# Kernel optimization log

Hardware: AMD Instinct MI355X
Metric: run time of the kernel (lower is better)

## Reference

```python
import jax, jax.numpy as jnp
import numpy as np

N, D, H, L = 50000, 128, 4, 3
E = 800000
C = D // H            # head dim = 32
NEG_SLOPE = 0.2       # PyG GATv2Conv default negative_slope
LN_EPS = 1e-5         # nn.LayerNorm default eps


def setup_inputs() -> dict:
    key = jax.random.key(0)
    ks = jax.random.split(key, 8)
    s = 1.0 / np.sqrt(D).astype(np.float32)
    return {
        "fine_poi_x": jax.random.normal(ks[0], (N, D), jnp.float32),
        "edge_index": jax.random.randint(ks[1], (2, E), 0, N, dtype=jnp.int32),
        "Wl": jax.random.normal(ks[2], (L, D, D), jnp.float32) * s,
        "bl": jnp.zeros((L, D), jnp.float32),
        "Wr": jax.random.normal(ks[3], (L, D, D), jnp.float32) * s,
        "br": jnp.zeros((L, D), jnp.float32),
        "att": jax.random.normal(ks[4], (L, H, C), jnp.float32) * s,
        "bias": jnp.zeros((L, D), jnp.float32),
        "gamma": jnp.ones((L, D), jnp.float32),
        "beta": jnp.zeros((L, D), jnp.float32),
    }


def _gatv2_conv(x, src, dst, Wl, bl, Wr, br, att, bias):
    # x: [N, D]; src/dst: [E'] (self-loops already appended)
    xl = (x @ Wl + bl).reshape(N, H, C)   # source-side transform (lin_l)
    xr = (x @ Wr + br).reshape(N, H, C)   # target-side transform (lin_r)
    m = xl[src] + xr[dst]                 # [E', H, C] per-edge pre-activation
    m = jax.nn.leaky_relu(m, NEG_SLOPE)
    e = jnp.einsum("ehc,hc->eh", m, att)  # [E', H] attention logits
    # segment softmax over edges grouped by destination node
    emax = jax.ops.segment_max(e, dst, num_segments=N)      # [N, H]
    ee = jnp.exp(e - emax[dst])
    denom = jax.ops.segment_sum(ee, dst, num_segments=N)    # [N, H]
    alpha = ee / denom[dst]               # self-loops guarantee denom >= 1 term
    out = jax.ops.segment_sum(xl[src] * alpha[:, :, None], dst, num_segments=N)
    return out.reshape(N, D) + bias


def _layernorm(x, g, b):
    mu = jnp.mean(x, axis=-1, keepdims=True)
    var = jnp.var(x, axis=-1, keepdims=True)
    return (x - mu) * jax.lax.rsqrt(var + LN_EPS) * g + b


def reference(fine_poi_x, edge_index, Wl, bl, Wr, br, att, bias, gamma, beta):
    # PyG GATv2Conv add_self_loops=True: append i->i edges
    loops = jnp.arange(N, dtype=edge_index.dtype)
    src = jnp.concatenate([edge_index[0], loops])
    dst = jnp.concatenate([edge_index[1], loops])
    x = fine_poi_x
    for i in range(L):
        h = _gatv2_conv(x, src, dst, Wl[i], bl[i], Wr[i], br[i], att[i], bias[i])
        x = _layernorm(x + h, gamma[i], beta[i])
        if i != L - 1:
            x = jax.nn.relu(x)
    return x
```

## Files before the change

kernel.cpp:

```cpp
#include <hip/hip_runtime.h>

#define N_NODES 50000
#define N_EDGES 800000
#define DIM 128
#define TOT_EDGES (N_EDGES + N_NODES)
#define LOG2E 1.44269504088896f

#define BSHIFT 9
#define BNODES 512
#define NB ((N_NODES + BNODES - 1) / BNODES)
#define BCAP 16384
#define EPB 4096
#define EPT 16
#define NBLK_A ((TOT_EDGES + EPB - 1) / EPB)

typedef __attribute__((ext_vector_type(8))) _Float16 f16x8;
typedef __attribute__((ext_vector_type(2))) _Float16 h2;
typedef __attribute__((ext_vector_type(4))) float f32x4;
typedef decltype(__builtin_amdgcn_cvt_pkrtz(0.f, 0.f)) fp16v2;

__device__ inline uint h2u(h2 v) { return __builtin_bit_cast(uint, v); }
__device__ inline h2 u2h(uint v) { return __builtin_bit_cast(h2, v); }
__device__ inline uint pk2u(fp16v2 v) { return __builtin_bit_cast(uint, v); }

__device__ inline float rowsum16(float v) {
  int x;
  x = __builtin_amdgcn_update_dpp(0, __float_as_int(v), 0x128, 0xF, 0xF, true);
  v += __int_as_float(x);
  x = __builtin_amdgcn_update_dpp(0, __float_as_int(v), 0x124, 0xF, 0xF, true);
  v += __int_as_float(x);
  x = __builtin_amdgcn_update_dpp(0, __float_as_int(v), 0x122, 0xF, 0xF, true);
  v += __int_as_float(x);
  x = __builtin_amdgcn_update_dpp(0, __float_as_int(v), 0x121, 0xF, 0xF, true);
  v += __int_as_float(x);
  return v;
}

__device__ inline float quadsum4(float v) {
  int x;
  x = __builtin_amdgcn_update_dpp(0, __float_as_int(v), 0xB1, 0xF, 0xF, true);
  v += __int_as_float(x);
  x = __builtin_amdgcn_update_dpp(0, __float_as_int(v), 0x4E, 0xF, 0xF, true);
  v += __int_as_float(x);
  return v;
}


__global__ __launch_bounds__(256) void convx_kernel(const float* __restrict__ x,
                                                    uint* __restrict__ xb,
                                                    int* __restrict__ bcnt) {
  if (blockIdx.x == 0 && threadIdx.x < NB) bcnt[threadIdx.x] = 0;
  int t = blockIdx.x * 256 + threadIdx.x;
  if (t < N_NODES * (DIM / 2)) {
    float2 v = ((const float2*)x)[t];
    xb[t] = pk2u(__builtin_amdgcn_cvt_pkrtz(v.x, v.y));
  }
}

__global__ __launch_bounds__(256) void convwa_kernel(const float* __restrict__ Wl,
                                                     const float* __restrict__ Wr,
                                                     ushort* __restrict__ Wt,
                                                     const float* __restrict__ att,
                                                     uint* __restrict__ attc,
                                                     uint* __restrict__ col) {
  int t = blockIdx.x * 256 + threadIdx.x;
  if (blockIdx.x == 0) {
    int u = threadIdx.x;
    if (u < 192) {
      float a0 = att[2 * u] * LOG2E, a1 = att[2 * u + 1] * LOG2E;
      attc[u] = pk2u(__builtin_amdgcn_cvt_pkrtz(a0, a1));
    }
    if (u < 64) col[TOT_EDGES + u] = 0u;
  }
  if (t >= 3 * 2 * DIM * DIM) return;
  int k = t & 127;
  int n = (t >> 7) & 127;
  int w = (t >> 14) & 1;
  int l = t >> 15;
  const float* W = w ? Wr : Wl;
  _Float16 h = (_Float16)W[l * DIM * DIM + k * DIM + n];
  Wt[t] = __builtin_bit_cast(ushort, h);
}


__global__ __launch_bounds__(256) void partA_kernel(const int* __restrict__ srcArr,
                                                    const int* __restrict__ dstArr,
                                                    int* __restrict__ bcnt,
                                                    uint2* __restrict__ bbuf) {
  int tid = threadIdx.x;
  int e0 = blockIdx.x * EPB;
  __shared__ int hist[NB], base[NB], loff[NB];
  if (tid < NB) { hist[tid] = 0; loff[tid] = 0; }
  __syncthreads();

  int sv[EPT], dv[EPT];
#pragma unroll
  for (int i = 0; i < EPT; ++i) {
    int e = e0 + i * 256 + tid;
    int s = 0, d = -1;
    if (e < TOT_EDGES) {
      if (e < N_EDGES) { s = srcArr[e]; d = dstArr[e]; }
      else { s = e - N_EDGES; d = s; }
    }
    sv[i] = s; dv[i] = d;
    if (d >= 0) atomicAdd(&hist[d >> BSHIFT], 1);
  }
  __syncthreads();
  if (tid < NB) {
    int h = hist[tid];
    if (h > 0) base[tid] = atomicAdd(&bcnt[tid], h);
  }
  __syncthreads();
#pragma unroll
  for (int i = 0; i < EPT; ++i) {
    int d = dv[i];
    if (d >= 0) {
      int b = d >> BSHIFT;
      int p = atomicAdd(&loff[b], 1);
      bbuf[(size_t)b * BCAP + base[b] + p] = make_uint2((uint)sv[i], (uint)d);
    }
  }
}


__global__ __launch_bounds__(512) void partB_kernel(const uint2* __restrict__ bbuf,
                                                    const int* __restrict__ bcnt,
                                                    int* __restrict__ rowptr,
                                                    uint* __restrict__ col) {
  int b = blockIdx.x, tid = threadIdx.x;

  __shared__ int s[128];
  if (tid < 128) s[tid] = (tid < NB) ? bcnt[tid] : 0;
  __syncthreads();
  for (int off = 1; off < 128; off <<= 1) {
    int t = 0;
    if (tid < 128 && tid >= off) t = s[tid - off];
    __syncthreads();
    if (tid < 128) s[tid] += t;
    __syncthreads();
  }
  int cb = (b > 0) ? s[b - 1] : 0;
  int m = bcnt[b];
  if (b == 0 && tid == 0) rowptr[N_NODES] = TOT_EDGES;
  const uint2* buf = bbuf + (size_t)b * BCAP;

  __shared__ int cnt[BNODES], scn[BNODES], cur[BNODES];
  cnt[tid] = 0;
  __syncthreads();
  for (int e = tid; e < m; e += 512) {
    int d = (int)buf[e].y;
    atomicAdd(&cnt[d & (BNODES - 1)], 1);
  }
  __syncthreads();
  int c = cnt[tid];
  scn[tid] = c;
  __syncthreads();
  for (int off = 1; off < BNODES; off <<= 1) {
    int t = (tid >= off) ? scn[tid - off] : 0;
    __syncthreads();
    scn[tid] += t;
    __syncthreads();
  }
  int excl = scn[tid] - c;
  int node = b * BNODES + tid;
  if (node < N_NODES) rowptr[node] = cb + excl;
  cur[tid] = excl;
  __syncthreads();
  for (int e = tid; e < m; e += 512) {
    uint2 sd = buf[e];
    int p = atomicAdd(&cur[(int)sd.y & (BNODES - 1)], 1);
    col[cb + p] = sd.x * 16u;
  }
}


__global__ __launch_bounds__(256) void gemm_mfma_kernel(
    const uint* __restrict__ xb,
    const ushort* __restrict__ Wt,
    const float* __restrict__ bl, const float* __restrict__ br,
    uint* __restrict__ xl, uint* __restrict__ xr) {
  int wave = threadIdx.x >> 6, lane = threadIdx.x & 63;
  int lr = lane & 15, kq = lane >> 4;
  int m0 = blockIdx.x * 64;

  const ushort* W = Wt + (wave >> 1) * (DIM * DIM);
  const float* bias = (wave >> 1) ? br : bl;
  uint* outp = (wave >> 1) ? xr : xl;
  int n0 = (wave & 1) * 64;
  const ushort* xbp = (const ushort*)xb;

  f16x8 bfrag[4][4];
#pragma unroll
  for (int nt = 0; nt < 4; ++nt)
#pragma unroll
    for (int kt = 0; kt < 4; ++kt)
      bfrag[nt][kt] = *(const f16x8*)(W + (n0 + nt * 16 + lr) * DIM + kt * 32 + kq * 8);

  f32x4 acc[4][4];
#pragma unroll
  for (int mt = 0; mt < 4; ++mt)
#pragma unroll
    for (int nt = 0; nt < 4; ++nt)
      acc[mt][nt] = (f32x4){0.f, 0.f, 0.f, 0.f};

  f16x8 af[4];
  {
    int m = m0 + lr;
    int mc = m < N_NODES ? m : N_NODES - 1;
#pragma unroll
    for (int kt = 0; kt < 4; ++kt)
      af[kt] = *(const f16x8*)(xbp + (size_t)mc * DIM + kt * 32 + kq * 8);
  }
#pragma unroll
  for (int mt = 0; mt < 4; ++mt) {
    f16x8 afn[4];
    if (mt < 3) {
      int m2 = m0 + (mt + 1) * 16 + lr;
      int mc2 = m2 < N_NODES ? m2 : N_NODES - 1;
#pragma unroll
      for (int kt = 0; kt < 4; ++kt)
        afn[kt] = *(const f16x8*)(xbp + (size_t)mc2 * DIM + kt * 32 + kq * 8);
    }
#pragma unroll
    for (int nt = 0; nt < 4; ++nt)
#pragma unroll
      for (int kt = 0; kt < 4; ++kt)
        acc[mt][nt] = __builtin_amdgcn_mfma_f32_16x16x32_f16(bfrag[nt][kt], af[kt],
                                                             acc[mt][nt], 0, 0, 0);
    if (mt < 3) {
      af[0] = afn[0]; af[1] = afn[1]; af[2] = afn[2]; af[3] = afn[3];
    }
  }

#pragma unroll
  for (int mt = 0; mt < 4; ++mt) {
    int m = m0 + mt * 16 + lr;
    if (m < N_NODES) {
#pragma unroll
      for (int nt = 0; nt < 4; ++nt) {
        int n = n0 + nt * 16 + kq * 4;
        float4 bb = *(const float4*)(bias + n);
        uint2 o;
        o.x = pk2u(__builtin_amdgcn_cvt_pkrtz(acc[mt][nt][0] + bb.x, acc[mt][nt][1] + bb.y));
        o.y = pk2u(__builtin_amdgcn_cvt_pkrtz(acc[mt][nt][2] + bb.z, acc[mt][nt][3] + bb.w));
        *(uint2*)(outp + (size_t)m * (DIM / 2) + (n >> 1)) = o;
      }
    }
  }
}


__global__ __launch_bounds__(64) void att_kernel(
    const uint4* __restrict__ xinb, const uint4* __restrict__ xlb,
    const uint4* __restrict__ xrb, const int* __restrict__ rowptr,
    const uint* __restrict__ col, const uint4* __restrict__ attc,
    const float4* __restrict__ bias, const float4* __restrict__ gamma,
    const float4* __restrict__ beta, uint4* __restrict__ xoutb,
    float4* __restrict__ xoutf, int do_relu) {
  int lane = threadIdx.x;
  uint j = (uint)(lane & 15);
  int e4 = lane >> 4;
  int n = blockIdx.x;

  uint4 rq = xrb[(uint)(n * 16) + j];
  uint4 aq = attc[j];
  h2 r2[4] = {u2h(rq.x), u2h(rq.y), u2h(rq.z), u2h(rq.w)};
  h2 at2[4] = {u2h(aq.x), u2h(aq.y), u2h(aq.z), u2h(aq.w)};
  const h2 c02 = {(_Float16)0.2f, (_Float16)0.2f};

  h2 accp[4] = {};
  float den = 0.f;

  int js = rowptr[n], je = rowptr[n + 1];

  uint cA = col[(uint)(js + e4)];
  uint cB = col[(uint)(js + 4 + e4)];
  uint cC = col[(uint)(js + 8 + e4)];
  uint4 gA = xlb[cA + j];
  uint4 gB = xlb[cB + j];

  for (int cbase = js; cbase < je; cbase += 4) {
    uint cD = col[(uint)(cbase + 12 + e4)];
    uint4 gC = xlb[cC + j];

    h2 a0 = u2h(gA.x), a1 = u2h(gA.y), a2 = u2h(gA.z), a3 = u2h(gA.w);
    float p = 0.f;
    {
      h2 s0 = a0 + r2[0], s1 = a1 + r2[1], s2 = a2 + r2[2], s3 = a3 + r2[3];
      h2 m0 = __builtin_elementwise_max(s0, s0 * c02);
      h2 m1 = __builtin_elementwise_max(s1, s1 * c02);
      h2 m2 = __builtin_elementwise_max(s2, s2 * c02);
      h2 m3 = __builtin_elementwise_max(s3, s3 * c02);
      p = __builtin_amdgcn_fdot2(__builtin_bit_cast(fp16v2, m0),
                                 __builtin_bit_cast(fp16v2, at2[0]), p, false);
      p = __builtin_amdgcn_fdot2(__builtin_bit_cast(fp16v2, m1),
                                 __builtin_bit_cast(fp16v2, at2[1]), p, false);
      p = __builtin_amdgcn_fdot2(__builtin_bit_cast(fp16v2, m2),
                                 __builtin_bit_cast(fp16v2, at2[2]), p, false);
      p = __builtin_amdgcn_fdot2(__builtin_bit_cast(fp16v2, m3),
                                 __builtin_bit_cast(fp16v2, at2[3]), p, false);
    }
    p = quadsum4(p);
    float w = (cbase + e4 < je) ? __builtin_amdgcn_exp2f(p) : 0.f;
    den += w;
    _Float16 wh = (_Float16)w;
    h2 w2 = {wh, wh};
    accp[0] = w2 * a0 + accp[0];
    accp[1] = w2 * a1 + accp[1];
    accp[2] = w2 * a2 + accp[2];
    accp[3] = w2 * a3 + accp[3];

    gA = gB; gB = gC; cC = cD;
  }

#pragma unroll
  for (int t = 0; t < 4; ++t) {
    accp[t] += u2h((uint)__shfl_xor((int)h2u(accp[t]), 16, 64));
    accp[t] += u2h((uint)__shfl_xor((int)h2u(accp[t]), 32, 64));
  }
  den += __shfl_xor(den, 16, 64);
  den += __shfl_xor(den, 32, 64);

  float inv = 1.0f / den;
  float acc[8];
#pragma unroll
  for (int t = 0; t < 4; ++t) {
    acc[2 * t] = (float)accp[t].x;
    acc[2 * t + 1] = (float)accp[t].y;
  }

  uint4 xi4 = xinb[(uint)(n * 16) + j];
  h2 xi[4] = {u2h(xi4.x), u2h(xi4.y), u2h(xi4.z), u2h(xi4.w)};
  float4 b0 = bias[2 * j], b1 = bias[2 * j + 1];

  float o[8];
  o[0] = fmaf(acc[0], inv, b0.x + (float)xi[0].x);
  o[1] = fmaf(acc[1], inv, b0.y + (float)xi[0].y);
  o[2] = fmaf(acc[2], inv, b0.z + (float)xi[1].x);
  o[3] = fmaf(acc[3], inv, b0.w + (float)xi[1].y);
  o[4] = fmaf(acc[4], inv, b1.x + (float)xi[2].x);
  o[5] = fmaf(acc[5], inv, b1.y + (float)xi[2].y);
  o[6] = fmaf(acc[6], inv, b1.z + (float)xi[3].x);
  o[7] = fmaf(acc[7], inv, b1.w + (float)xi[3].y);

  float s1 = 0.f, s2 = 0.f;
#pragma unroll
  for (int t = 0; t < 8; ++t) { s1 += o[t]; s2 = fmaf(o[t], o[t], s2); }
  s1 = rowsum16(s1);
  s2 = rowsum16(s2);
  float mean = s1 * (1.0f / DIM);
  float var = s2 * (1.0f / DIM) - mean * mean;
  float rstd = rsqrtf(var + 1e-5f);

  float4 g0 = gamma[2 * j], g1 = gamma[2 * j + 1];
  float4 t0 = beta[2 * j], t1 = beta[2 * j + 1];
  float y[8];
  y[0] = (o[0] - mean) * rstd * g0.x + t0.x;
  y[1] = (o[1] - mean) * rstd * g0.y + t0.y;
  y[2] = (o[2] - mean) * rstd * g0.z + t0.z;
  y[3] = (o[3] - mean) * rstd * g0.w + t0.w;
  y[4] = (o[4] - mean) * rstd * g1.x + t1.x;
  y[5] = (o[5] - mean) * rstd * g1.y + t1.y;
  y[6] = (o[6] - mean) * rstd * g1.z + t1.z;
  y[7] = (o[7] - mean) * rstd * g1.w + t1.w;
  if (do_relu) {
#pragma unroll
    for (int t = 0; t < 8; ++t) y[t] = fmaxf(y[t], 0.f);
  }

  if (e4 == 0) {
    if (xoutb) {
      uint4 ov;
      ov.x = pk2u(__builtin_amdgcn_cvt_pkrtz(y[0], y[1]));
      ov.y = pk2u(__builtin_amdgcn_cvt_pkrtz(y[2], y[3]));
      ov.z = pk2u(__builtin_amdgcn_cvt_pkrtz(y[4], y[5]));
      ov.w = pk2u(__builtin_amdgcn_cvt_pkrtz(y[6], y[7]));
      xoutb[(uint)(n * 16) + j] = ov;
    }
    if (xoutf) {
      xoutf[(uint)(n * 32) + 2 * j] = make_float4(y[0], y[1], y[2], y[3]);
      xoutf[(uint)(n * 32) + 2 * j + 1] = make_float4(y[4], y[5], y[6], y[7]);
    }
  }
}


extern "C" void kernel_launch(void* const* d_in, const int* in_sizes, int n_in,
                              void* d_out, int out_size, void* d_ws, size_t ws_size,
                              hipStream_t stream) {
  const float* x_in  = (const float*)d_in[0];
  const int*   eidx  = (const int*)d_in[1];
  const float* Wl    = (const float*)d_in[2];
  const float* bl    = (const float*)d_in[3];
  const float* Wr    = (const float*)d_in[4];
  const float* br    = (const float*)d_in[5];
  const float* att   = (const float*)d_in[6];
  const float* bias  = (const float*)d_in[7];
  const float* gamma = (const float*)d_in[8];
  const float* beta  = (const float*)d_in[9];
  float* out = (float*)d_out;

  char* p = (char*)d_ws;
  auto alloc = [&](size_t bytes) {
    char* q = p;
    p += (bytes + 255) & ~(size_t)255;
    return q;
  };
  uint*  xb       = (uint*)alloc((size_t)N_NODES * (DIM / 2) * 4);
  uint*  xlb      = (uint*)alloc((size_t)N_NODES * (DIM / 2) * 4);
  uint*  xrb      = (uint*)alloc((size_t)N_NODES * (DIM / 2) * 4);
  ushort* Wt      = (ushort*)alloc((size_t)3 * 2 * DIM * DIM * 2);
  uint*  attc     = (uint*)alloc((size_t)3 * 64 * 4);
  int*   rowptr   = (int*)alloc((size_t)(N_NODES + 1) * 4);
  uint*  col      = (uint*)alloc((size_t)(TOT_EDGES + 64) * 4);
  uint2* bbuf     = (uint2*)alloc((size_t)NB * BCAP * 8);
  int*   bcnt     = (int*)alloc((size_t)NB * 4);

  convx_kernel<<<(N_NODES * (DIM / 2) + 255) / 256, 256, 0, stream>>>(x_in, xb, bcnt);
  convwa_kernel<<<(3 * 2 * DIM * DIM + 255) / 256, 256, 0, stream>>>(Wl, Wr, Wt, att, attc, col);
  partA_kernel<<<NBLK_A, 256, 0, stream>>>(eidx, eidx + N_EDGES, bcnt, bbuf);
  partB_kernel<<<NB, 512, 0, stream>>>(bbuf, bcnt, rowptr, col);

  for (int l = 0; l < 3; ++l) {
    gemm_mfma_kernel<<<(N_NODES + 63) / 64, 256, 0, stream>>>(
        xb, Wt + (size_t)l * 2 * DIM * DIM, bl + l * DIM, br + l * DIM, xlb, xrb);
    att_kernel<<<N_NODES, 64, 0, stream>>>(
        (const uint4*)xb, (const uint4*)xlb, (const uint4*)xrb, rowptr, col,
        (const uint4*)(attc + l * 64), (const float4*)(bias + l * DIM),
        (const float4*)(gamma + l * DIM), (const float4*)(beta + l * DIM),
        (l == 2) ? nullptr : (uint4*)xb, (l == 2) ? (float4*)out : nullptr,
        (l != 2) ? 1 : 0);
  }
}
```

Baseline: 240.0 us.

## Merge conversion kernels, pack bucket entries into 32 bits, deepen gather prefetch

Merges the x and weight conversion kernels into a single launch by splitting the grid between the two jobs. Bucket-partition entries are packed into one 32-bit word (source index shifted left by 9, local destination in the low bits), which halves the bbuf write and read traffic. The attention kernel's gather pipeline is deepened from two to five rows of xl in flight, with col indices fetched further ahead, to hide gather latency. The deeper prefetch costs more registers and reads further past each node's edge range. Those extra reads now extend up to 28 entries past the edge array, while only 64 padding entries are zeroed.

```diff
diff --git a/kernel.cpp b/kernel.cpp
--- a/kernel.cpp
+++ b/kernel.cpp
@@ -13,6 +13,8 @@
 #define EPB 4096
 #define EPT 16
 #define NBLK_A ((TOT_EDGES + EPB - 1) / EPB)
+#define CONVX_BLOCKS ((N_NODES * (DIM / 2) + 255) / 256)
+#define CONVW_BLOCKS ((3 * 2 * DIM * DIM + 255) / 256)
 
 typedef __attribute__((ext_vector_type(8))) _Float16 f16x8;
 typedef __attribute__((ext_vector_type(2))) _Float16 h2;
@@ -46,47 +48,51 @@
 }
 
 
-__global__ __launch_bounds__(256) void convx_kernel(const float* __restrict__ x,
-                                                    uint* __restrict__ xb,
-                                                    int* __restrict__ bcnt) {
-  if (blockIdx.x == 0 && threadIdx.x < NB) bcnt[threadIdx.x] = 0;
-  int t = blockIdx.x * 256 + threadIdx.x;
-  if (t < N_NODES * (DIM / 2)) {
-    float2 v = ((const float2*)x)[t];
-    xb[t] = pk2u(__builtin_amdgcn_cvt_pkrtz(v.x, v.y));
-  }
-}
-
-__global__ __launch_bounds__(256) void convwa_kernel(const float* __restrict__ Wl,
-                                                     const float* __restrict__ Wr,
-                                                     ushort* __restrict__ Wt,
-                                                     const float* __restrict__ att,
-                                                     uint* __restrict__ attc,
-                                                     uint* __restrict__ col) {
-  int t = blockIdx.x * 256 + threadIdx.x;
-  if (blockIdx.x == 0) {
-    int u = threadIdx.x;
-    if (u < 192) {
-      float a0 = att[2 * u] * LOG2E, a1 = att[2 * u + 1] * LOG2E;
-      attc[u] = pk2u(__builtin_amdgcn_cvt_pkrtz(a0, a1));
-    }
-    if (u < 64) col[TOT_EDGES + u] = 0u;
-  }
-  if (t >= 3 * 2 * DIM * DIM) return;
-  int k = t & 127;
-  int n = (t >> 7) & 127;
-  int w = (t >> 14) & 1;
-  int l = t >> 15;
-  const float* W = w ? Wr : Wl;
-  _Float16 h = (_Float16)W[l * DIM * DIM + k * DIM + n];
-  Wt[t] = __builtin_bit_cast(ushort, h);
+__global__ __launch_bounds__(256) void conv_kernel(const float* __restrict__ x,
+                                                   uint* __restrict__ xb,
+                                                   int* __restrict__ bcnt,
+                                                   const float* __restrict__ Wl,
+                                                   const float* __restrict__ Wr,
+                                                   ushort* __restrict__ Wt,
+                                                   const float* __restrict__ att,
+                                                   uint* __restrict__ attc,
+                                                   uint* __restrict__ col) {
+  int b = blockIdx.x;
+  if (b < CONVX_BLOCKS) {
+    if (b == 0 && threadIdx.x < NB) bcnt[threadIdx.x] = 0;
+    int t = b * 256 + threadIdx.x;
+    if (t < N_NODES * (DIM / 2)) {
+      float2 v = ((const float2*)x)[t];
+      xb[t] = pk2u(__builtin_amdgcn_cvt_pkrtz(v.x, v.y));
+    }
+  } else {
+    int bb = b - CONVX_BLOCKS;
+    if (bb == 0) {
+      int u = threadIdx.x;
+      if (u < 192) {
+        float a0 = att[2 * u] * LOG2E, a1 = att[2 * u + 1] * LOG2E;
+        attc[u] = pk2u(__builtin_amdgcn_cvt_pkrtz(a0, a1));
+      }
+      if (u < 64) col[TOT_EDGES + u] = 0u;
+    }
+    int t = bb * 256 + threadIdx.x;
+    if (t < 3 * 2 * DIM * DIM) {
+      int k = t & 127;
+      int n = (t >> 7) & 127;
+      int w = (t >> 14) & 1;
+      int l = t >> 15;
+      const float* W = w ? Wr : Wl;
+      _Float16 h = (_Float16)W[l * DIM * DIM + k * DIM + n];
+      Wt[t] = __builtin_bit_cast(ushort, h);
+    }
+  }
 }
 
 
 __global__ __launch_bounds__(256) void partA_kernel(const int* __restrict__ srcArr,
                                                     const int* __restrict__ dstArr,
                                                     int* __restrict__ bcnt,
-                                                    uint2* __restrict__ bbuf) {
+                                                    uint* __restrict__ bbuf) {
   int tid = threadIdx.x;
   int e0 = blockIdx.x * EPB;
   __shared__ int hist[NB], base[NB], loff[NB];
@@ -117,13 +123,13 @@
     if (d >= 0) {
       int b = d >> BSHIFT;
       int p = atomicAdd(&loff[b], 1);
-      bbuf[(size_t)b * BCAP + base[b] + p] = make_uint2((uint)sv[i], (uint)d);
-    }
-  }
-}
-
-
-__global__ __launch_bounds__(512) void partB_kernel(const uint2* __restrict__ bbuf,
+      bbuf[(size_t)b * BCAP + base[b] + p] = ((uint)sv[i] << 9) | (uint)(d & (BNODES - 1));
+    }
+  }
+}
+
+
+__global__ __launch_bounds__(512) void partB_kernel(const uint* __restrict__ bbuf,
                                                     const int* __restrict__ bcnt,
                                                     int* __restrict__ rowptr,
                                                     uint* __restrict__ col) {
@@ -142,14 +148,13 @@
   int cb = (b > 0) ? s[b - 1] : 0;
   int m = bcnt[b];
   if (b == 0 && tid == 0) rowptr[N_NODES] = TOT_EDGES;
-  const uint2* buf = bbuf + (size_t)b * BCAP;
+  const uint* buf = bbuf + (size_t)b * BCAP;
 
   __shared__ int cnt[BNODES], scn[BNODES], cur[BNODES];
   cnt[tid] = 0;
   __syncthreads();
   for (int e = tid; e < m; e += 512) {
-    int d = (int)buf[e].y;
-    atomicAdd(&cnt[d & (BNODES - 1)], 1);
+    atomicAdd(&cnt[buf[e] & (BNODES - 1)], 1);
   }
   __syncthreads();
   int c = cnt[tid];
@@ -167,9 +172,9 @@
   cur[tid] = excl;
   __syncthreads();
   for (int e = tid; e < m; e += 512) {
-    uint2 sd = buf[e];
-    int p = atomicAdd(&cur[(int)sd.y & (BNODES - 1)], 1);
-    col[cb + p] = sd.x * 16u;
+    uint sd = buf[e];
+    int p = atomicAdd(&cur[sd & (BNODES - 1)], 1);
+    col[cb + p] = (sd >> 9) << 4;
   }
 }
 
@@ -273,17 +278,24 @@
 
   int js = rowptr[n], je = rowptr[n + 1];
 
-  uint cA = col[(uint)(js + e4)];
-  uint cB = col[(uint)(js + 4 + e4)];
-  uint cC = col[(uint)(js + 8 + e4)];
-  uint4 gA = xlb[cA + j];
-  uint4 gB = xlb[cB + j];
+  uint c0 = col[(uint)(js + e4)];
+  uint c1 = col[(uint)(js + 4 + e4)];
+  uint c2 = col[(uint)(js + 8 + e4)];
+  uint c3 = col[(uint)(js + 12 + e4)];
+  uint c4 = col[(uint)(js + 16 + e4)];
+  uint c5 = col[(uint)(js + 20 + e4)];
+  uint c6 = col[(uint)(js + 24 + e4)];
+  uint4 g0 = xlb[c0 + j];
+  uint4 g1 = xlb[c1 + j];
+  uint4 g2 = xlb[c2 + j];
+  uint4 g3 = xlb[c3 + j];
+  uint4 g4 = xlb[c4 + j];
 
   for (int cbase = js; cbase < je; cbase += 4) {
-    uint cD = col[(uint)(cbase + 12 + e4)];
-    uint4 gC = xlb[cC + j];
-
-    h2 a0 = u2h(gA.x), a1 = u2h(gA.y), a2 = u2h(gA.z), a3 = u2h(gA.w);
+    uint cn = col[(uint)(cbase + 28 + e4)];
+    uint4 gn = xlb[c5 + j];
+
+    h2 a0 = u2h(g0.x), a1 = u2h(g0.y), a2 = u2h(g0.z), a3 = u2h(g0.w);
     float p = 0.f;
     {
       h2 s0 = a0 + r2[0], s1 = a1 + r2[1], s2 = a2 + r2[2], s3 = a3 + r2[3];
@@ -310,7 +322,8 @@
     accp[2] = w2 * a2 + accp[2];
     accp[3] = w2 * a3 + accp[3];
 
-    gA = gB; gB = gC; cC = cD;
+    g0 = g1; g1 = g2; g2 = g3; g3 = g4; g4 = gn;
+    c5 = c6; c6 = cn;
   }
 
 #pragma unroll
@@ -352,17 +365,17 @@
   float var = s2 * (1.0f / DIM) - mean * mean;
   float rstd = rsqrtf(var + 1e-5f);
 
-  float4 g0 = gamma[2 * j], g1 = gamma[2 * j + 1];
+  float4 g0_ = gamma[2 * j], g1_ = gamma[2 * j + 1];
   float4 t0 = beta[2 * j], t1 = beta[2 * j + 1];
   float y[8];
-  y[0] = (o[0] - mean) * rstd * g0.x + t0.x;
-  y[1] = (o[1] - mean) * rstd * g0.y + t0.y;
-  y[2] = (o[2] - mean) * rstd * g0.z + t0.z;
-  y[3] = (o[3] - mean) * rstd * g0.w + t0.w;
-  y[4] = (o[4] - mean) * rstd * g1.x + t1.x;
-  y[5] = (o[5] - mean) * rstd * g1.y + t1.y;
-  y[6] = (o[6] - mean) * rstd * g1.z + t1.z;
-  y[7] = (o[7] - mean) * rstd * g1.w + t1.w;
+  y[0] = (o[0] - mean) * rstd * g0_.x + t0.x;
+  y[1] = (o[1] - mean) * rstd * g0_.y + t0.y;
+  y[2] = (o[2] - mean) * rstd * g0_.z + t0.z;
+  y[3] = (o[3] - mean) * rstd * g0_.w + t0.w;
+  y[4] = (o[4] - mean) * rstd * g1_.x + t1.x;
+  y[5] = (o[5] - mean) * rstd * g1_.y + t1.y;
+  y[6] = (o[6] - mean) * rstd * g1_.z + t1.z;
+  y[7] = (o[7] - mean) * rstd * g1_.w + t1.w;
   if (do_relu) {
 #pragma unroll
     for (int t = 0; t < 8; ++t) y[t] = fmaxf(y[t], 0.f);
@@ -413,11 +426,11 @@
   uint*  attc     = (uint*)alloc((size_t)3 * 64 * 4);
   int*   rowptr   = (int*)alloc((size_t)(N_NODES + 1) * 4);
   uint*  col      = (uint*)alloc((size_t)(TOT_EDGES + 64) * 4);
-  uint2* bbuf     = (uint2*)alloc((size_t)NB * BCAP * 8);
+  uint*  bbuf     = (uint*)alloc((size_t)NB * BCAP * 4);
   int*   bcnt     = (int*)alloc((size_t)NB * 4);
 
-  convx_kernel<<<(N_NODES * (DIM / 2) + 255) / 256, 256, 0, stream>>>(x_in, xb, bcnt);
-  convwa_kernel<<<(3 * 2 * DIM * DIM + 255) / 256, 256, 0, stream>>>(Wl, Wr, Wt, att, attc, col);
+  conv_kernel<<<CONVX_BLOCKS + CONVW_BLOCKS, 256, 0, stream>>>(
+      x_in, xb, bcnt, Wl, Wr, Wt, att, attc, col);
   partA_kernel<<<NBLK_A, 256, 0, stream>>>(eidx, eidx + N_EDGES, bcnt, bbuf);
   partB_kernel<<<NB, 512, 0, stream>>>(bbuf, bcnt, rowptr, col);
 
```

Measured after the change: 238.9 us (median of 2 runs). Within noise of the previous version (-0.4%).
